# Kernel tuning notes

Measured on AMD Instinct MI355X. Metric: run time of the kernel, lower is better.

The kernel has to match this reference:

```python
import jax, jax.numpy as jnp
from jax import lax
import numpy as np

LATENT = 16
HIDDEN = 16  # latent_dim > 8 -> 16
NUM_ATTRACTORS = 64
GRAVITY = 0.01
INPUT_DIM = 300
B, S = 32, 2048
N_ITERS = 20


def setup_inputs() -> dict:
    key = jax.random.key(0)
    ks = jax.random.split(key, 12)
    sc = lambda fan_in: 1.0 / np.sqrt(fan_in)
    return {
        "inputs": jax.random.normal(ks[0], (B, S, INPUT_DIM), dtype=jnp.float32),
        "enc_w1": jax.random.normal(ks[1], (INPUT_DIM, HIDDEN), dtype=jnp.float32) * sc(INPUT_DIM),
        "enc_b1": jnp.zeros((HIDDEN,), dtype=jnp.float32),
        "enc_w2": jax.random.normal(ks[2], (HIDDEN, LATENT), dtype=jnp.float32) * sc(HIDDEN),
        "enc_b2": jnp.zeros((LATENT,), dtype=jnp.float32),
        "attractors": jax.random.normal(ks[3], (NUM_ATTRACTORS, LATENT), dtype=jnp.float32) * 0.1,
        "dec_w1": jax.random.normal(ks[4], (LATENT, HIDDEN), dtype=jnp.float32) * sc(LATENT),
        "dec_b1": jnp.zeros((HIDDEN,), dtype=jnp.float32),
        "dec_w2": jax.random.normal(ks[5], (HIDDEN, INPUT_DIM), dtype=jnp.float32) * sc(HIDDEN),
        "dec_b2": jnp.zeros((INPUT_DIM,), dtype=jnp.float32),
        "mass_w": jax.random.normal(ks[6], (LATENT, 1), dtype=jnp.float32) * sc(LATENT),
        "mass_b": jnp.zeros((1,), dtype=jnp.float32),
    }


def reference(inputs, enc_w1, enc_b1, enc_w2, enc_b2, attractors,
              dec_w1, dec_b1, dec_w2, dec_b2, mass_w, mass_b):
    b, s, _ = inputs.shape
    # encoder: Linear(300,16) -> ReLU -> Linear(16,latent)
    h = jax.nn.relu(jnp.einsum('bsi,ih->bsh', inputs, enc_w1) + enc_b1)
    emb = jnp.einsum('bsh,hd->bsd', h, enc_w2) + enc_b2  # [B,S,D]

    def step(pos, _):
        # pos: [B,S,D]; attractors: [A,D]
        diff = attractors[None, None, :, :] - pos[:, :, None, :]          # [B,S,A,D]
        dist = jnp.sqrt(jnp.sum(diff * diff, axis=-1, keepdims=True)) + 1e-6
        forces = jnp.sum(GRAVITY * diff / (dist * dist), axis=2)          # [B,S,D]
        new_pos = pos + 0.1 * forces
        change = jnp.sqrt(jnp.sum((new_pos - pos) ** 2))
        return new_pos, change

    # torch code breaks if change < 1e-6; with random data this never fires,
    # so the fixed 20-iteration scan is equivalent.
    positions, changes = lax.scan(step, emb, None, length=N_ITERS)

    attractor_field = positions.mean(axis=1)                              # [B,D]
    rec = jax.nn.relu(attractor_field @ dec_w1 + dec_b1) @ dec_w2 + dec_b2  # [B,300]
    reconstructions = jnp.broadcast_to(rec[:, None, :], (b, s, INPUT_DIM))
    masses = jax.nn.sigmoid(attractor_field @ mass_w + mass_b)            # [B,1]
    final_change = changes[-1]
    return attractor_field, reconstructions, masses, final_change
```

## Files before the change

### kernel.cpp

```cpp
#include <hip/hip_runtime.h>
#include <cmath>

#define BB 32
#define SS 2048
#define IND 300
#define HID 16
#define LAT 16
#define NA 64
#define NITER 20
#define GRAV 0.01f

#define OFF_FIELD 0
#define OFF_REC   512
#define OFF_MASS  (512 + BB*SS*IND)
#define OFF_CHG   (OFF_MASS + BB)

#define WS_FIELD 0
#define WS_CHG   512

typedef __attribute__((ext_vector_type(8))) __bf16 bf16x8;
typedef __attribute__((ext_vector_type(4))) __bf16 bf16x4;
typedef __attribute__((ext_vector_type(2))) __bf16 bf16x2;
typedef __attribute__((ext_vector_type(4))) float f32x4;
typedef __attribute__((ext_vector_type(4))) unsigned uint4v;

#define HST 40

__device__ __forceinline__ unsigned pk_bf16(float lo, float hi) {
    bf16x2 t; t[0] = (__bf16)lo; t[1] = (__bf16)hi;
    return __builtin_bit_cast(unsigned, t);
}

__global__ __launch_bounds__(256, 4)
void k_fused(const float* __restrict__ x,  const float* __restrict__ w1,
             const float* __restrict__ b1, const float* __restrict__ w2,
             const float* __restrict__ b2, const float* __restrict__ att,
             float* __restrict__ ws)
{
    __shared__ __align__(16) __bf16 hl[4][16 * HST];
    __shared__ float red[4][LAT];
    __shared__ float redc[4];

    const int tid  = threadIdx.x;
    const int wave = tid >> 6, lane = tid & 63;
    const int quad = lane >> 4, col = lane & 15;
    const int tok  = blockIdx.x * 64 + wave * 16 + col;

    f32x4 p;
    {
        const float* xr = x + (size_t)tok * IND;

        f32x4 xv[10][2];
        #pragma unroll
        for (int s = 0; s < 9; ++s) {
            const float* xp = xr + s * 32 + quad * 8;
            xv[s][0] = *(const f32x4*)(xp);
            xv[s][1] = *(const f32x4*)(xp + 4);
        }
        {
            const f32x4 z = {0.f, 0.f, 0.f, 0.f};
            xv[9][0] = z; xv[9][1] = z;
            if (quad == 0) {
                xv[9][0] = *(const f32x4*)(xr + 288);
                xv[9][1] = *(const f32x4*)(xr + 292);
            } else if (quad == 1) {
                xv[9][0] = *(const f32x4*)(xr + 296);
            }
        }

        const float b1c = b1[col];
        f32x4 hacc = {b1c, b1c, b1c, b1c};
        #pragma unroll
        for (int s = 0; s < 10; ++s) {
            bf16x8 af, wf;
            #pragma unroll
            for (int e = 0; e < 4; ++e) {
                af[e]     = (__bf16)xv[s][0][e];
                af[4 + e] = (__bf16)xv[s][1][e];
            }
            if (s < 9) {
                #pragma unroll
                for (int j = 0; j < 8; ++j)
                    wf[j] = (__bf16)w1[(s * 32 + quad * 8 + j) * HID + col];
            } else {
                #pragma unroll
                for (int j = 0; j < 8; ++j)
                    wf[j] = (quad * 8 + j < 12)
                          ? (__bf16)w1[(288 + quad * 8 + j) * HID + col]
                          : (__bf16)0.f;
            }
            hacc = __builtin_amdgcn_mfma_f32_16x16x32_bf16(af, wf, hacc, 0, 0, 0);
        }

        __bf16* myh = hl[wave];
        #pragma unroll
        for (int r = 0; r < 4; ++r)
            myh[(quad * 4 + r) * HST + col] = (__bf16)fmaxf(hacc[r], 0.f);

        bf16x8 w2tf;
        #pragma unroll
        for (int j = 0; j < 8; ++j) {
            const int k = quad * 8 + j;
            w2tf[j] = (k < HID) ? (__bf16)w2[k * LAT + col] : (__bf16)0.f;
        }
        bf16x8 bh;
        #pragma unroll
        for (int e = 0; e < 8; ++e) bh[e] = (__bf16)0.f;
        if (quad < 2)
            bh = *(const bf16x8*)(myh + col * HST + quad * 8);
        f32x4 pacc = *(const f32x4*)(b2 + quad * 4);
        p = __builtin_amdgcn_mfma_f32_16x16x32_bf16(w2tf, bh, pacc, 0, 0, 0);
    }

    const f32x4 zf = {0.f, 0.f, 0.f, 0.f};
    bf16x8 ones8;
    #pragma unroll
    for (int e = 0; e < 8; ++e) ones8[e] = (__bf16)1.0f;

    bf16x8 aS[4];
    #pragma unroll
    for (int i = 0; i < 4; ++i) {
        f32x4 av = *(const f32x4*)(att + (16 * i + col) * LAT + quad * 4);
        #pragma unroll
        for (int m = 0; m < 4; ++m) {
            aS[i][2 * m]     = (__bf16)(-2.0f * av[m]);
            aS[i][2 * m + 1] = (__bf16)1.0f;
        }
    }
    f32x4 sanv[4];
    {
        float nrm[4];
        #pragma unroll
        for (int i = 0; i < 4; ++i) {
            const float* ar = att + (16 * i + col) * LAT;
            float s = 0.f;
            #pragma unroll
            for (int k = 0; k < LAT; ++k) s = fmaf(ar[k], ar[k], s);
            nrm[i] = s;
        }
        #pragma unroll
        for (int i = 0; i < 4; ++i)
            #pragma unroll
            for (int r = 0; r < 4; ++r)
                sanv[i][r] = __shfl(nrm[i], 16 * quad + quad * 4 + r);
    }
    bf16x8 aF[2];
    #pragma unroll
    for (int h = 0; h < 2; ++h)
        #pragma unroll
        for (int j = 0; j < 8; ++j)
            aF[h][j] = (__bf16)att[(32 * h + quad * 8 + j) * LAT + col];

    const int bpA0 = (((quad & 1) * 32) + col) * 4;
    const int bpA1 = bpA0 + 64;
    const bool qhi = (quad & 2) != 0;

    float cd = 0.f;
    #pragma unroll 1
    for (int it = 0; it < NITER; ++it) {
        bf16x8 bp;
        #pragma unroll
        for (int m = 0; m < 4; ++m) {
            float v = p[m];
            bp[2 * m]     = (__bf16)v;
            bp[2 * m + 1] = (__bf16)(v * v);
        }
        f32x4 sf[4];
        #pragma unroll
        for (int i = 0; i < 4; ++i)
            sf[i] = __builtin_amdgcn_mfma_f32_16x16x32_bf16(aS[i], bp, zf, 0, 0, 0);

        unsigned sd0[4], sd1[4];
        #pragma unroll
        for (int i = 0; i < 4; ++i) {
            float w0 = __builtin_amdgcn_rcpf(sf[i][0] + sanv[i][0]);
            float w1_ = __builtin_amdgcn_rcpf(sf[i][1] + sanv[i][1]);
            float w2_ = __builtin_amdgcn_rcpf(sf[i][2] + sanv[i][2]);
            float w3_ = __builtin_amdgcn_rcpf(sf[i][3] + sanv[i][3]);
            sd0[i] = pk_bf16(w0, w1_);
            sd1[i] = pk_bf16(w2_, w3_);
        }
        unsigned ra0 = qhi ? sd0[1] : sd0[0];
        unsigned rb0 = qhi ? sd1[1] : sd1[0];
        unsigned ra1 = qhi ? sd0[3] : sd0[2];
        unsigned rb1 = qhi ? sd1[3] : sd1[2];

        int b0 = __builtin_amdgcn_ds_bpermute(bpA0, (int)ra0);
        int b1v = __builtin_amdgcn_ds_bpermute(bpA0, (int)rb0);
        int b2v = __builtin_amdgcn_ds_bpermute(bpA1, (int)ra0);
        int b3 = __builtin_amdgcn_ds_bpermute(bpA1, (int)rb0);
        int b4 = __builtin_amdgcn_ds_bpermute(bpA0, (int)ra1);
        int b5 = __builtin_amdgcn_ds_bpermute(bpA0, (int)rb1);
        int b6 = __builtin_amdgcn_ds_bpermute(bpA1, (int)ra1);
        int b7 = __builtin_amdgcn_ds_bpermute(bpA1, (int)rb1);

        uint4v u0 = {(unsigned)b0, (unsigned)b1v, (unsigned)b2v, (unsigned)b3};
        uint4v u1 = {(unsigned)b4, (unsigned)b5, (unsigned)b6, (unsigned)b7};
        bf16x8 bw0 = __builtin_bit_cast(bf16x8, u0);
        bf16x8 bw1 = __builtin_bit_cast(bf16x8, u1);

        f32x4 F  = __builtin_amdgcn_mfma_f32_16x16x32_bf16(aF[0], bw0, zf, 0, 0, 0);
        F  = __builtin_amdgcn_mfma_f32_16x16x32_bf16(aF[1], bw1, F,  0, 0, 0);
        f32x4 F2 = __builtin_amdgcn_mfma_f32_16x16x32_bf16(ones8, bw0, zf, 0, 0, 0);
        F2 = __builtin_amdgcn_mfma_f32_16x16x32_bf16(ones8, bw1, F2, 0, 0, 0);

        const bool last = (it == NITER - 1);
        #pragma unroll
        for (int r = 0; r < 4; ++r) {
            float np = fmaf(p[r], fmaf(F2[r], -0.1f * GRAV, 1.0f),
                            (0.1f * GRAV) * F[r]);
            if (last) { float d = np - p[r]; cd = fmaf(d, d, cd); }
            p[r] = np;
        }
    }

    f32x4 fs = p;
    #pragma unroll
    for (int m = 1; m <= 8; m <<= 1)
        #pragma unroll
        for (int r = 0; r < 4; ++r) fs[r] += __shfl_xor(fs[r], m);
    if (col == 0) {
        #pragma unroll
        for (int r = 0; r < 4; ++r) red[wave][quad * 4 + r] = fs[r];
    }
    float c2 = cd;
    c2 += __shfl_xor(c2, 1);  c2 += __shfl_xor(c2, 2);  c2 += __shfl_xor(c2, 4);
    c2 += __shfl_xor(c2, 8);  c2 += __shfl_xor(c2, 16); c2 += __shfl_xor(c2, 32);
    if (lane == 0) redc[wave] = c2;
    __syncthreads();

    const int b = blockIdx.x >> 5;
    if (tid < LAT) {
        float v = red[0][tid] + red[1][tid] + red[2][tid] + red[3][tid];
        atomicAdd(ws + WS_FIELD + b * LAT + tid, v);
    }
    if (tid == 32)
        atomicAdd(ws + WS_CHG + (blockIdx.x & 63),
                  redc[0] + redc[1] + redc[2] + redc[3]);
}

#define CHUNK 8192
#define CPB   (SS * IND / CHUNK)
__global__ __launch_bounds__(256)
void k_bcast(const float* __restrict__ dw1, const float* __restrict__ db1,
             const float* __restrict__ dw2, const float* __restrict__ db2,
             const float* __restrict__ mw,  const float* __restrict__ mb,
             const float* __restrict__ ws, float* __restrict__ out)
{
    __shared__ float sf[LAT];
    __shared__ float sh[HID];
    __shared__ float schg[64];
    __shared__ __align__(16) float srow[IND];
    const int blk = blockIdx.x;
    const int b = blk / CPB, c = blk % CPB;
    const int t = threadIdx.x;

    if (t < LAT) {
        float f = ws[WS_FIELD + b * LAT + t] * (1.f / SS);
        sf[t] = f;
        if (c == 0) out[OFF_FIELD + b * LAT + t] = f;
    }
    if (blk == 0 && t < 64) schg[t] = ws[WS_CHG + t];
    __syncthreads();
    if (t < HID) {
        float a = db1[t];
        #pragma unroll
        for (int d = 0; d < LAT; ++d) a = fmaf(sf[d], dw1[d * HID + t], a);
        sh[t] = fmaxf(a, 0.f);
    }
    if (c == 0 && t == 32) {
        float a = mb[0];
        #pragma unroll
        for (int d = 0; d < LAT; ++d) a = fmaf(sf[d], mw[d], a);
        out[OFF_MASS + b] = 1.f / (1.f + expf(-a));
    }
    if (blk == 0 && t == 33) {
        float s = 0.f;
        #pragma unroll
        for (int i = 0; i < 64; ++i) s += schg[i];
        out[OFF_CHG] = sqrtf(s);
    }
    __syncthreads();
    if (t < IND) {
        float a = db2[t];
        #pragma unroll
        for (int j = 0; j < HID; ++j) a = fmaf(sh[j], dw2[j * IND + t], a);
        srow[t] = a;
    }
    if (t < IND - 256) {
        const int tc = t + 256;
        float a2 = db2[tc];
        #pragma unroll
        for (int j = 0; j < HID; ++j) a2 = fmaf(sh[j], dw2[j * IND + tc], a2);
        srow[tc] = a2;
    }
    __syncthreads();
    f32x4* o = (f32x4*)(out + OFF_REC + (size_t)b * (SS * IND) + (size_t)c * CHUNK);
    #pragma unroll
    for (int i = 0; i < CHUNK / 4 / 256; ++i) {
        const int o4 = i * 256 + t;
        const int r  = (c * CHUNK + o4 * 4) % IND;
        f32x4 v = *(const f32x4*)(srow + r);
        __builtin_nontemporal_store(v, o + o4);
    }
}

extern "C" void kernel_launch(void* const* d_in, const int* in_sizes, int n_in,
                              void* d_out, int out_size, void* d_ws, size_t ws_size,
                              hipStream_t stream)
{
    const float* x   = (const float*)d_in[0];
    const float* ew1 = (const float*)d_in[1];
    const float* eb1 = (const float*)d_in[2];
    const float* ew2 = (const float*)d_in[3];
    const float* eb2 = (const float*)d_in[4];
    const float* att = (const float*)d_in[5];
    const float* dw1 = (const float*)d_in[6];
    const float* db1 = (const float*)d_in[7];
    const float* dw2 = (const float*)d_in[8];
    const float* db2 = (const float*)d_in[9];
    const float* mw  = (const float*)d_in[10];
    const float* mb  = (const float*)d_in[11];
    float* out = (float*)d_out;
    float* ws  = (float*)d_ws;

    (void)hipMemsetAsync(ws, 0, (WS_CHG + 64) * sizeof(float), stream);
    k_fused<<<BB * SS / 64, 256, 0, stream>>>(x, ew1, eb1, ew2, eb2, att, ws);
    k_bcast<<<BB * CPB, 256, 0, stream>>>(dw1, db1, dw2, db2, mw, mb, ws, out);
}
```

Baseline: 192.9 us.

## Process two 16-token tiles per wave to interleave independent MFMA chains

Each wave now handles 32 tokens as two independent 16-token tiles. The encoder loads, encoder MFMAs and the 20-iteration attractor loop are interleaved across the two tiles, so their dependency chains can overlap and hide MFMA, rcp and bpermute latency. The grid is halved, launch bounds drop to 2 blocks per CU, and the batch index mapping is adjusted to match. The cost is higher register pressure (two sets of 20 x-vectors, doubled accumulators), lower occupancy and fewer blocks in flight.

```diff
diff --git a/kernel.cpp b/kernel.cpp
--- a/kernel.cpp
+++ b/kernel.cpp
@@ -31,53 +31,50 @@
     return __builtin_bit_cast(unsigned, t);
 }
 
-__global__ __launch_bounds__(256, 4)
+__global__ __launch_bounds__(256, 2)
 void k_fused(const float* __restrict__ x,  const float* __restrict__ w1,
              const float* __restrict__ b1, const float* __restrict__ w2,
              const float* __restrict__ b2, const float* __restrict__ att,
              float* __restrict__ ws)
 {
-    __shared__ __align__(16) __bf16 hl[4][16 * HST];
+    __shared__ __align__(16) __bf16 hl[4][2][16 * HST];
     __shared__ float red[4][LAT];
     __shared__ float redc[4];
 
     const int tid  = threadIdx.x;
     const int wave = tid >> 6, lane = tid & 63;
     const int quad = lane >> 4, col = lane & 15;
-    const int tok  = blockIdx.x * 64 + wave * 16 + col;
-
-    f32x4 p;
+    const int tok0 = blockIdx.x * 128 + wave * 32 + col;
+
+    f32x4 p[2];
     {
-        const float* xr = x + (size_t)tok * IND;
-
-        f32x4 xv[10][2];
-        #pragma unroll
-        for (int s = 0; s < 9; ++s) {
-            const float* xp = xr + s * 32 + quad * 8;
-            xv[s][0] = *(const f32x4*)(xp);
-            xv[s][1] = *(const f32x4*)(xp + 4);
-        }
-        {
+        f32x4 xv[2][10][2];
+        #pragma unroll
+        for (int t2 = 0; t2 < 2; ++t2) {
+            const float* xr = x + (size_t)(tok0 + 16 * t2) * IND;
+            #pragma unroll
+            for (int s = 0; s < 9; ++s) {
+                const float* xp = xr + s * 32 + quad * 8;
+                xv[t2][s][0] = *(const f32x4*)(xp);
+                xv[t2][s][1] = *(const f32x4*)(xp + 4);
+            }
             const f32x4 z = {0.f, 0.f, 0.f, 0.f};
-            xv[9][0] = z; xv[9][1] = z;
+            xv[t2][9][0] = z; xv[t2][9][1] = z;
             if (quad == 0) {
-                xv[9][0] = *(const f32x4*)(xr + 288);
-                xv[9][1] = *(const f32x4*)(xr + 292);
+                xv[t2][9][0] = *(const f32x4*)(xr + 288);
+                xv[t2][9][1] = *(const f32x4*)(xr + 292);
             } else if (quad == 1) {
-                xv[9][0] = *(const f32x4*)(xr + 296);
-            }
-        }
+                xv[t2][9][0] = *(const f32x4*)(xr + 296);
+            }
+        }
+        __builtin_amdgcn_sched_barrier(0);
 
         const float b1c = b1[col];
-        f32x4 hacc = {b1c, b1c, b1c, b1c};
+        f32x4 haccA = {b1c, b1c, b1c, b1c};
+        f32x4 haccB = {b1c, b1c, b1c, b1c};
         #pragma unroll
         for (int s = 0; s < 10; ++s) {
-            bf16x8 af, wf;
-            #pragma unroll
-            for (int e = 0; e < 4; ++e) {
-                af[e]     = (__bf16)xv[s][0][e];
-                af[4 + e] = (__bf16)xv[s][1][e];
-            }
+            bf16x8 wf;
             if (s < 9) {
                 #pragma unroll
                 for (int j = 0; j < 8; ++j)
@@ -89,13 +86,23 @@
                           ? (__bf16)w1[(288 + quad * 8 + j) * HID + col]
                           : (__bf16)0.f;
             }
-            hacc = __builtin_amdgcn_mfma_f32_16x16x32_bf16(af, wf, hacc, 0, 0, 0);
-        }
-
-        __bf16* myh = hl[wave];
-        #pragma unroll
-        for (int r = 0; r < 4; ++r)
-            myh[(quad * 4 + r) * HST + col] = (__bf16)fmaxf(hacc[r], 0.f);
+            bf16x8 afA, afB;
+            #pragma unroll
+            for (int e = 0; e < 4; ++e) {
+                afA[e]     = (__bf16)xv[0][s][0][e];
+                afA[4 + e] = (__bf16)xv[0][s][1][e];
+                afB[e]     = (__bf16)xv[1][s][0][e];
+                afB[4 + e] = (__bf16)xv[1][s][1][e];
+            }
+            haccA = __builtin_amdgcn_mfma_f32_16x16x32_bf16(afA, wf, haccA, 0, 0, 0);
+            haccB = __builtin_amdgcn_mfma_f32_16x16x32_bf16(afB, wf, haccB, 0, 0, 0);
+        }
+
+        #pragma unroll
+        for (int r = 0; r < 4; ++r) {
+            hl[wave][0][(quad * 4 + r) * HST + col] = (__bf16)fmaxf(haccA[r], 0.f);
+            hl[wave][1][(quad * 4 + r) * HST + col] = (__bf16)fmaxf(haccB[r], 0.f);
+        }
 
         bf16x8 w2tf;
         #pragma unroll
@@ -103,13 +110,16 @@
             const int k = quad * 8 + j;
             w2tf[j] = (k < HID) ? (__bf16)w2[k * LAT + col] : (__bf16)0.f;
         }
-        bf16x8 bh;
-        #pragma unroll
-        for (int e = 0; e < 8; ++e) bh[e] = (__bf16)0.f;
-        if (quad < 2)
-            bh = *(const bf16x8*)(myh + col * HST + quad * 8);
-        f32x4 pacc = *(const f32x4*)(b2 + quad * 4);
-        p = __builtin_amdgcn_mfma_f32_16x16x32_bf16(w2tf, bh, pacc, 0, 0, 0);
+        const f32x4 pacc = *(const f32x4*)(b2 + quad * 4);
+        #pragma unroll
+        for (int t2 = 0; t2 < 2; ++t2) {
+            bf16x8 bh;
+            #pragma unroll
+            for (int e = 0; e < 8; ++e) bh[e] = (__bf16)0.f;
+            if (quad < 2)
+                bh = *(const bf16x8*)(&hl[wave][t2][0] + col * HST + quad * 8);
+            p[t2] = __builtin_amdgcn_mfma_f32_16x16x32_bf16(w2tf, bh, pacc, 0, 0, 0);
+        }
     }
 
     const f32x4 zf = {0.f, 0.f, 0.f, 0.f};
@@ -158,63 +168,68 @@
     float cd = 0.f;
     #pragma unroll 1
     for (int it = 0; it < NITER; ++it) {
-        bf16x8 bp;
-        #pragma unroll
-        for (int m = 0; m < 4; ++m) {
-            float v = p[m];
-            bp[2 * m]     = (__bf16)v;
-            bp[2 * m + 1] = (__bf16)(v * v);
-        }
-        f32x4 sf[4];
-        #pragma unroll
-        for (int i = 0; i < 4; ++i)
-            sf[i] = __builtin_amdgcn_mfma_f32_16x16x32_bf16(aS[i], bp, zf, 0, 0, 0);
-
-        unsigned sd0[4], sd1[4];
-        #pragma unroll
-        for (int i = 0; i < 4; ++i) {
-            float w0 = __builtin_amdgcn_rcpf(sf[i][0] + sanv[i][0]);
-            float w1_ = __builtin_amdgcn_rcpf(sf[i][1] + sanv[i][1]);
-            float w2_ = __builtin_amdgcn_rcpf(sf[i][2] + sanv[i][2]);
-            float w3_ = __builtin_amdgcn_rcpf(sf[i][3] + sanv[i][3]);
-            sd0[i] = pk_bf16(w0, w1_);
-            sd1[i] = pk_bf16(w2_, w3_);
-        }
-        unsigned ra0 = qhi ? sd0[1] : sd0[0];
-        unsigned rb0 = qhi ? sd1[1] : sd1[0];
-        unsigned ra1 = qhi ? sd0[3] : sd0[2];
-        unsigned rb1 = qhi ? sd1[3] : sd1[2];
-
-        int b0 = __builtin_amdgcn_ds_bpermute(bpA0, (int)ra0);
-        int b1v = __builtin_amdgcn_ds_bpermute(bpA0, (int)rb0);
-        int b2v = __builtin_amdgcn_ds_bpermute(bpA1, (int)ra0);
-        int b3 = __builtin_amdgcn_ds_bpermute(bpA1, (int)rb0);
-        int b4 = __builtin_amdgcn_ds_bpermute(bpA0, (int)ra1);
-        int b5 = __builtin_amdgcn_ds_bpermute(bpA0, (int)rb1);
-        int b6 = __builtin_amdgcn_ds_bpermute(bpA1, (int)ra1);
-        int b7 = __builtin_amdgcn_ds_bpermute(bpA1, (int)rb1);
-
-        uint4v u0 = {(unsigned)b0, (unsigned)b1v, (unsigned)b2v, (unsigned)b3};
-        uint4v u1 = {(unsigned)b4, (unsigned)b5, (unsigned)b6, (unsigned)b7};
-        bf16x8 bw0 = __builtin_bit_cast(bf16x8, u0);
-        bf16x8 bw1 = __builtin_bit_cast(bf16x8, u1);
-
-        f32x4 F  = __builtin_amdgcn_mfma_f32_16x16x32_bf16(aF[0], bw0, zf, 0, 0, 0);
-        F  = __builtin_amdgcn_mfma_f32_16x16x32_bf16(aF[1], bw1, F,  0, 0, 0);
-        f32x4 F2 = __builtin_amdgcn_mfma_f32_16x16x32_bf16(ones8, bw0, zf, 0, 0, 0);
-        F2 = __builtin_amdgcn_mfma_f32_16x16x32_bf16(ones8, bw1, F2, 0, 0, 0);
-
-        const bool last = (it == NITER - 1);
-        #pragma unroll
-        for (int r = 0; r < 4; ++r) {
-            float np = fmaf(p[r], fmaf(F2[r], -0.1f * GRAV, 1.0f),
-                            (0.1f * GRAV) * F[r]);
-            if (last) { float d = np - p[r]; cd = fmaf(d, d, cd); }
-            p[r] = np;
-        }
-    }
-
-    f32x4 fs = p;
+        #pragma unroll
+        for (int t2 = 0; t2 < 2; ++t2) {
+            bf16x8 bp;
+            #pragma unroll
+            for (int m = 0; m < 4; ++m) {
+                float v = p[t2][m];
+                bp[2 * m]     = (__bf16)v;
+                bp[2 * m + 1] = (__bf16)(v * v);
+            }
+            f32x4 sf[4];
+            #pragma unroll
+            for (int i = 0; i < 4; ++i)
+                sf[i] = __builtin_amdgcn_mfma_f32_16x16x32_bf16(aS[i], bp, zf, 0, 0, 0);
+
+            unsigned sd0[4], sd1[4];
+            #pragma unroll
+            for (int i = 0; i < 4; ++i) {
+                float w0  = __builtin_amdgcn_rcpf(sf[i][0] + sanv[i][0]);
+                float w1_ = __builtin_amdgcn_rcpf(sf[i][1] + sanv[i][1]);
+                float w2_ = __builtin_amdgcn_rcpf(sf[i][2] + sanv[i][2]);
+                float w3_ = __builtin_amdgcn_rcpf(sf[i][3] + sanv[i][3]);
+                sd0[i] = pk_bf16(w0, w1_);
+                sd1[i] = pk_bf16(w2_, w3_);
+            }
+            unsigned ra0 = qhi ? sd0[1] : sd0[0];
+            unsigned rb0 = qhi ? sd1[1] : sd1[0];
+            unsigned ra1 = qhi ? sd0[3] : sd0[2];
+            unsigned rb1 = qhi ? sd1[3] : sd1[2];
+
+            int b0  = __builtin_amdgcn_ds_bpermute(bpA0, (int)ra0);
+            int b1v = __builtin_amdgcn_ds_bpermute(bpA0, (int)rb0);
+            int b2v = __builtin_amdgcn_ds_bpermute(bpA1, (int)ra0);
+            int b3  = __builtin_amdgcn_ds_bpermute(bpA1, (int)rb0);
+            int b4  = __builtin_amdgcn_ds_bpermute(bpA0, (int)ra1);
+            int b5  = __builtin_amdgcn_ds_bpermute(bpA0, (int)rb1);
+            int b6  = __builtin_amdgcn_ds_bpermute(bpA1, (int)ra1);
+            int b7  = __builtin_amdgcn_ds_bpermute(bpA1, (int)rb1);
+
+            uint4v u0 = {(unsigned)b0, (unsigned)b1v, (unsigned)b2v, (unsigned)b3};
+            uint4v u1 = {(unsigned)b4, (unsigned)b5, (unsigned)b6, (unsigned)b7};
+            bf16x8 bw0 = __builtin_bit_cast(bf16x8, u0);
+            bf16x8 bw1 = __builtin_bit_cast(bf16x8, u1);
+
+            f32x4 F  = __builtin_amdgcn_mfma_f32_16x16x32_bf16(aF[0], bw0, zf, 0, 0, 0);
+            F  = __builtin_amdgcn_mfma_f32_16x16x32_bf16(aF[1], bw1, F,  0, 0, 0);
+            f32x4 F2 = __builtin_amdgcn_mfma_f32_16x16x32_bf16(ones8, bw0, zf, 0, 0, 0);
+            F2 = __builtin_amdgcn_mfma_f32_16x16x32_bf16(ones8, bw1, F2, 0, 0, 0);
+
+            const bool last = (it == NITER - 1);
+            #pragma unroll
+            for (int r = 0; r < 4; ++r) {
+                float np = fmaf(p[t2][r], fmaf(F2[r], -0.1f * GRAV, 1.0f),
+                                (0.1f * GRAV) * F[r]);
+                if (last) { float d = np - p[t2][r]; cd = fmaf(d, d, cd); }
+                p[t2][r] = np;
+            }
+        }
+    }
+
+    f32x4 fs;
+    #pragma unroll
+    for (int r = 0; r < 4; ++r) fs[r] = p[0][r] + p[1][r];
     #pragma unroll
     for (int m = 1; m <= 8; m <<= 1)
         #pragma unroll
@@ -229,7 +244,7 @@
     if (lane == 0) redc[wave] = c2;
     __syncthreads();
 
-    const int b = blockIdx.x >> 5;
+    const int b = blockIdx.x >> 4;
     if (tid < LAT) {
         float v = red[0][tid] + red[1][tid] + red[2][tid] + red[3][tid];
         atomicAdd(ws + WS_FIELD + b * LAT + tid, v);
@@ -325,6 +340,6 @@
     float* ws  = (float*)d_ws;
 
     (void)hipMemsetAsync(ws, 0, (WS_CHG + 64) * sizeof(float), stream);
-    k_fused<<<BB * SS / 64, 256, 0, stream>>>(x, ew1, eb1, ew2, eb2, att, ws);
+    k_fused<<<BB * SS / 128, 256, 0, stream>>>(x, ew1, eb1, ew2, eb2, att, ws);
     k_bcast<<<BB * CPB, 256, 0, stream>>>(dw1, db1, dw2, db2, mw, mb, ws, out);
 }
```

After: 191.6 us. Within noise of the previous version (-0.7%).

## Permute attractor rows to eliminate per-iteration bpermute shuffles and hoist input loads

Applied to the files above, without the earlier changes.

Reorders the attractor rows feeding the score MFMA so each lane's reciprocal outputs already sit in the B-operand layout of the force MFMA. This removes eight ds_bpermute ops and the selects from every iteration. The precomputed norms are permuted to match. Input row loads are also issued before the attractor setup, with a sched_barrier, so global load latency overlaps that setup, at the cost of holding the loaded values in more registers.

```diff
diff --git a/kernel.cpp b/kernel.cpp
--- a/kernel.cpp
+++ b/kernel.cpp
@@ -46,28 +46,79 @@
     const int quad = lane >> 4, col = lane & 15;
     const int tok  = blockIdx.x * 64 + wave * 16 + col;
 
+    const float* xr = x + (size_t)tok * IND;
+    f32x4 xv[10][2];
+    #pragma unroll
+    for (int s = 0; s < 5; ++s) {
+        const float* xp = xr + s * 32 + quad * 8;
+        xv[s][0] = *(const f32x4*)(xp);
+        xv[s][1] = *(const f32x4*)(xp + 4);
+    }
+    __builtin_amdgcn_sched_barrier(0x7);
+    #pragma unroll
+    for (int s = 5; s < 9; ++s) {
+        const float* xp = xr + s * 32 + quad * 8;
+        xv[s][0] = *(const f32x4*)(xp);
+        xv[s][1] = *(const f32x4*)(xp + 4);
+    }
+    {
+        const f32x4 z = {0.f, 0.f, 0.f, 0.f};
+        xv[9][0] = z; xv[9][1] = z;
+        if (quad == 0) {
+            xv[9][0] = *(const f32x4*)(xr + 288);
+            xv[9][1] = *(const f32x4*)(xr + 292);
+        } else if (quad == 1) {
+            xv[9][0] = *(const f32x4*)(xr + 296);
+        }
+    }
+
+    const f32x4 zf = {0.f, 0.f, 0.f, 0.f};
+    bf16x8 ones8;
+    #pragma unroll
+    for (int e = 0; e < 8; ++e) ones8[e] = (__bf16)1.0f;
+
+    bf16x8 aS[4];
+    #pragma unroll
+    for (int i = 0; i < 4; ++i) {
+        const int arow = 32 * (i >> 1) + 8 * (col >> 2) + 4 * (i & 1) + (col & 3);
+        f32x4 av = *(const f32x4*)(att + arow * LAT + quad * 4);
+        #pragma unroll
+        for (int m = 0; m < 4; ++m) {
+            aS[i][2 * m]     = (__bf16)(-2.0f * av[m]);
+            aS[i][2 * m + 1] = (__bf16)1.0f;
+        }
+    }
+    f32x4 sanvP[4];
+    {
+        float nrm[4];
+        #pragma unroll
+        for (int i0 = 0; i0 < 4; ++i0) {
+            const float* ar = att + (16 * i0 + col) * LAT;
+            float s = 0.f;
+            #pragma unroll
+            for (int k = 0; k < LAT; ++k) s = fmaf(ar[k], ar[k], s);
+            nrm[i0] = s;
+        }
+        float nrmSel[2];
+        nrmSel[0] = (quad & 2) ? nrm[1] : nrm[0];
+        nrmSel[1] = (quad & 2) ? nrm[3] : nrm[2];
+        #pragma unroll
+        for (int i = 0; i < 4; ++i)
+            #pragma unroll
+            for (int r = 0; r < 4; ++r) {
+                const int src = (quad << 4) | (8 * (quad & 1) + 4 * (i & 1) + r);
+                sanvP[i][r] = __shfl(nrmSel[i >> 1], src);
+            }
+    }
+    bf16x8 aF[2];
+    #pragma unroll
+    for (int h = 0; h < 2; ++h)
+        #pragma unroll
+        for (int j = 0; j < 8; ++j)
+            aF[h][j] = (__bf16)att[(32 * h + quad * 8 + j) * LAT + col];
+
     f32x4 p;
     {
-        const float* xr = x + (size_t)tok * IND;
-
-        f32x4 xv[10][2];
-        #pragma unroll
-        for (int s = 0; s < 9; ++s) {
-            const float* xp = xr + s * 32 + quad * 8;
-            xv[s][0] = *(const f32x4*)(xp);
-            xv[s][1] = *(const f32x4*)(xp + 4);
-        }
-        {
-            const f32x4 z = {0.f, 0.f, 0.f, 0.f};
-            xv[9][0] = z; xv[9][1] = z;
-            if (quad == 0) {
-                xv[9][0] = *(const f32x4*)(xr + 288);
-                xv[9][1] = *(const f32x4*)(xr + 292);
-            } else if (quad == 1) {
-                xv[9][0] = *(const f32x4*)(xr + 296);
-            }
-        }
-
         const float b1c = b1[col];
         f32x4 hacc = {b1c, b1c, b1c, b1c};
         #pragma unroll
@@ -112,49 +163,6 @@
         p = __builtin_amdgcn_mfma_f32_16x16x32_bf16(w2tf, bh, pacc, 0, 0, 0);
     }
 
-    const f32x4 zf = {0.f, 0.f, 0.f, 0.f};
-    bf16x8 ones8;
-    #pragma unroll
-    for (int e = 0; e < 8; ++e) ones8[e] = (__bf16)1.0f;
-
-    bf16x8 aS[4];
-    #pragma unroll
-    for (int i = 0; i < 4; ++i) {
-        f32x4 av = *(const f32x4*)(att + (16 * i + col) * LAT + quad * 4);
-        #pragma unroll
-        for (int m = 0; m < 4; ++m) {
-            aS[i][2 * m]     = (__bf16)(-2.0f * av[m]);
-            aS[i][2 * m + 1] = (__bf16)1.0f;
-        }
-    }
-    f32x4 sanv[4];
-    {
-        float nrm[4];
-        #pragma unroll
-        for (int i = 0; i < 4; ++i) {
-            const float* ar = att + (16 * i + col) * LAT;
-            float s = 0.f;
-            #pragma unroll
-            for (int k = 0; k < LAT; ++k) s = fmaf(ar[k], ar[k], s);
-            nrm[i] = s;
-        }
-        #pragma unroll
-        for (int i = 0; i < 4; ++i)
-            #pragma unroll
-            for (int r = 0; r < 4; ++r)
-                sanv[i][r] = __shfl(nrm[i], 16 * quad + quad * 4 + r);
-    }
-    bf16x8 aF[2];
-    #pragma unroll
-    for (int h = 0; h < 2; ++h)
-        #pragma unroll
-        for (int j = 0; j < 8; ++j)
-            aF[h][j] = (__bf16)att[(32 * h + quad * 8 + j) * LAT + col];
-
-    const int bpA0 = (((quad & 1) * 32) + col) * 4;
-    const int bpA1 = bpA0 + 64;
-    const bool qhi = (quad & 2) != 0;
-
     float cd = 0.f;
     #pragma unroll 1
     for (int it = 0; it < NITER; ++it) {
@@ -170,32 +178,17 @@
         for (int i = 0; i < 4; ++i)
             sf[i] = __builtin_amdgcn_mfma_f32_16x16x32_bf16(aS[i], bp, zf, 0, 0, 0);
 
-        unsigned sd0[4], sd1[4];
-        #pragma unroll
-        for (int i = 0; i < 4; ++i) {
-            float w0 = __builtin_amdgcn_rcpf(sf[i][0] + sanv[i][0]);
-            float w1_ = __builtin_amdgcn_rcpf(sf[i][1] + sanv[i][1]);
-            float w2_ = __builtin_amdgcn_rcpf(sf[i][2] + sanv[i][2]);
-            float w3_ = __builtin_amdgcn_rcpf(sf[i][3] + sanv[i][3]);
-            sd0[i] = pk_bf16(w0, w1_);
-            sd1[i] = pk_bf16(w2_, w3_);
-        }
-        unsigned ra0 = qhi ? sd0[1] : sd0[0];
-        unsigned rb0 = qhi ? sd1[1] : sd1[0];
-        unsigned ra1 = qhi ? sd0[3] : sd0[2];
-        unsigned rb1 = qhi ? sd1[3] : sd1[2];
-
-        int b0 = __builtin_amdgcn_ds_bpermute(bpA0, (int)ra0);
-        int b1v = __builtin_amdgcn_ds_bpermute(bpA0, (int)rb0);
-        int b2v = __builtin_amdgcn_ds_bpermute(bpA1, (int)ra0);
-        int b3 = __builtin_amdgcn_ds_bpermute(bpA1, (int)rb0);
-        int b4 = __builtin_amdgcn_ds_bpermute(bpA0, (int)ra1);
-        int b5 = __builtin_amdgcn_ds_bpermute(bpA0, (int)rb1);
-        int b6 = __builtin_amdgcn_ds_bpermute(bpA1, (int)ra1);
-        int b7 = __builtin_amdgcn_ds_bpermute(bpA1, (int)rb1);
-
-        uint4v u0 = {(unsigned)b0, (unsigned)b1v, (unsigned)b2v, (unsigned)b3};
-        uint4v u1 = {(unsigned)b4, (unsigned)b5, (unsigned)b6, (unsigned)b7};
+        float w[4][4];
+        #pragma unroll
+        for (int i = 0; i < 4; ++i)
+            #pragma unroll
+            for (int r = 0; r < 4; ++r)
+                w[i][r] = __builtin_amdgcn_rcpf(sf[i][r] + sanvP[i][r]);
+
+        uint4v u0 = { pk_bf16(w[0][0], w[0][1]), pk_bf16(w[0][2], w[0][3]),
+                      pk_bf16(w[1][0], w[1][1]), pk_bf16(w[1][2], w[1][3]) };
+        uint4v u1 = { pk_bf16(w[2][0], w[2][1]), pk_bf16(w[2][2], w[2][3]),
+                      pk_bf16(w[3][0], w[3][1]), pk_bf16(w[3][2], w[3][3]) };
         bf16x8 bw0 = __builtin_bit_cast(bf16x8, u0);
         bf16x8 bw1 = __builtin_bit_cast(bf16x8, u1);
 
```

New measurement: 191.8 us. Within noise of the previous version (-0.6%).
